# Kernel tuning notes

Measured on AMD Instinct MI355X. Metric: run time of the kernel, lower is better.

The kernel has to match this reference:

```python
import jax, jax.numpy as jnp
import numpy as np

H = 512  # hidden_size


def setup_inputs() -> dict:
    key = jax.random.key(0)
    k1, k2, k3, k4, k5, k6 = jax.random.split(key, 6)
    B, S = 32, 2048
    output = jax.random.normal(k1, (B, H), dtype=jnp.float32)
    encoder_outputs = jax.random.normal(k2, (B, S, 2 * H), dtype=jnp.float32)
    encoder_mask = jax.random.randint(k3, (B, S), 0, 2, dtype=jnp.int32)
    # nn.Linear(3H, H): weight [H, 3H], bias [H]
    bound = 1.0 / np.sqrt(3 * H)
    W_attn = jax.random.uniform(k4, (H, 3 * H), minval=-bound, maxval=bound, dtype=jnp.float32)
    b_attn = jax.random.uniform(k5, (H,), minval=-bound, maxval=bound, dtype=jnp.float32)
    v = jax.random.normal(k6, (H,), dtype=jnp.float32) * (1.0 / np.sqrt(H))
    return {"output": output, "encoder_outputs": encoder_outputs,
            "encoder_mask": encoder_mask, "W_attn": W_attn, "b_attn": b_attn, "v": v}


def reference(output, encoder_outputs, encoder_mask, W_attn, b_attn, v):
    # Equivalent to cat([repeat(output), enc], -1) @ W.T: split W into state/enc blocks
    W_s = W_attn[:, :H]        # [H, H]   acts on decoder state
    W_e = W_attn[:, H:]        # [H, 2H]  acts on encoder outputs
    state_proj = output @ W_s.T                              # [B, H]
    enc_proj = jnp.einsum('bse,he->bsh', encoder_outputs, W_e)  # [B, S, H]
    energy = jnp.tanh(state_proj[:, None, :] + enc_proj + b_attn)  # [B, S, H]
    scores = jnp.einsum('bsh,h->bs', energy, v)[:, None, :]   # [B, 1, S]
    scores = scores - 1000.0 * (encoder_mask[:, None, :] == 0).astype(scores.dtype)
    return jax.nn.softmax(scores, axis=2)
```

## Files before the change

kernel.cpp:

```cpp
#include <hip/hip_runtime.h>
#include <hip/hip_bf16.h>

typedef __attribute__((ext_vector_type(4))) float f32x4;
typedef __attribute__((ext_vector_type(8))) short short8;

#define HH 512
#define BB 32
#define SS 2048
#define KK 1024

__device__ __forceinline__ unsigned short f2bf(float f) {
    unsigned int u = __float_as_uint(f);
    u += 0x7fffu + ((u >> 16) & 1u);
    return (unsigned short)(u >> 16);
}

__device__ __forceinline__ ushort4 pack4(float4 f) {
    ushort4 p;
    p.x = f2bf(f.x); p.y = f2bf(f.y); p.z = f2bf(f.z); p.w = f2bf(f.w);
    return p;
}

__device__ __forceinline__ float fast_tanh(float x) {
    float e = __expf(2.0f * x);
    return 1.0f - 2.0f / (e + 1.0f);
}

__global__ __launch_bounds__(256)
void spb_kernel(const float* __restrict__ out_state,
                const float* __restrict__ W,
                const float* __restrict__ bias,
                float* __restrict__ spb) {
    int wave = threadIdx.x >> 6, lane = threadIdx.x & 63;
    int g = blockIdx.x * 4 + wave;
    int b = g >> 9, h = g & 511;
    const float* wr = W + (size_t)h * 1536;
    const float* ov = out_state + b * HH;
    float4 w0 = *(const float4*)(wr + lane * 8);
    float4 w1 = *(const float4*)(wr + lane * 8 + 4);
    float4 o0 = *(const float4*)(ov + lane * 8);
    float4 o1 = *(const float4*)(ov + lane * 8 + 4);
    float d = w0.x * o0.x + w0.y * o0.y + w0.z * o0.z + w0.w * o0.w
            + w1.x * o1.x + w1.y * o1.y + w1.z * o1.z + w1.w * o1.w;
    d += __shfl_xor(d, 1); d += __shfl_xor(d, 2); d += __shfl_xor(d, 4);
    d += __shfl_xor(d, 8); d += __shfl_xor(d, 16); d += __shfl_xor(d, 32);
    if (lane == 0) spb[g] = d + bias[h];
}

__global__ void wconv_kernel(const float* __restrict__ W, unsigned short* __restrict__ Wt) {
    int idx = blockIdx.x * 256 + threadIdx.x;
    int e8 = idx * 8;
    int h = e8 >> 10;
    int k = e8 & 1023;
    const float* src = W + (size_t)h * 1536 + 512 + k;
    float4 w0 = *(const float4*)src;
    float4 w1 = *(const float4*)(src + 4);
    int kt = k >> 5;
    int q  = (k >> 3) & 3;
    int g  = h >> 4;
    int r  = h & 15;
    int ln = (q << 4) | r;
    unsigned short* dst = Wt + (size_t)kt * 16384 + g * 512 + ln * 8;
    *(ushort4*)dst = pack4(w0);
    *(ushort4*)(dst + 4) = pack4(w1);
}

__global__ __launch_bounds__(512, 4)
void attn_gemm(const float* __restrict__ enc, const unsigned short* __restrict__ Wt,
               const float* __restrict__ spb, const float* __restrict__ vvec,
               float* __restrict__ scores) {
    __shared__ unsigned short Asm[2 * 8192];
    __shared__ float red[8][64];

    const int tid = threadIdx.x;
    const int w = tid >> 6;
    const int lane = tid & 63;
    const int r = lane & 15;
    const int q = lane >> 4;
    const int b = blockIdx.x >> 5;
    const int s0 = (blockIdx.x & 31) << 6;

    const int arow = tid >> 3;
    const int akq = tid & 7;
    const float* arowp = enc + ((size_t)(b * SS + s0 + arow)) * KK + akq * 4;
    const int st_off = tid * 4;
    const int rd_off = r * 32 + q * 8;
    const unsigned short* wbase = Wt + (size_t)w * 2048 + lane * 8;

    f32x4 acc[4][4] = {};
    float4 f[4];

    #pragma unroll
    for (int t = 0; t < 4; ++t) f[t] = *(const float4*)(arowp + t * 32);
    #pragma unroll
    for (int t = 0; t < 4; ++t)
        *(ushort4*)(Asm + t * 2048 + st_off) = pack4(f[t]);
    __syncthreads();

    for (int p = 0; p < 8; ++p) {
        const int buf = p & 1;
        if (p < 7) {
            const float* src = arowp + (p + 1) * 128;
            #pragma unroll
            for (int t = 0; t < 4; ++t) f[t] = *(const float4*)(src + t * 32);
        }
        #pragma unroll
        for (int sub = 0; sub < 4; ++sub) {
            const int kt = p * 4 + sub;
            const short8* wp = (const short8*)(wbase + (size_t)kt * 16384);
            short8 bf[4];
            #pragma unroll
            for (int nf = 0; nf < 4; ++nf) bf[nf] = wp[nf * 64];
            const short8* ap = (const short8*)(Asm + buf * 8192 + sub * 2048 + rd_off);
            short8 af[4];
            #pragma unroll
            for (int mt = 0; mt < 4; ++mt) af[mt] = ap[mt * 64];
            #pragma unroll
            for (int mt = 0; mt < 4; ++mt)
                #pragma unroll
                for (int nf = 0; nf < 4; ++nf)
                    acc[mt][nf] = __builtin_amdgcn_mfma_f32_16x16x32_bf16(
                        af[mt], bf[nf], acc[mt][nf], 0, 0, 0);
        }
        if (p < 7) {
            unsigned short* dst = Asm + (buf ^ 1) * 8192 + st_off;
            #pragma unroll
            for (int t = 0; t < 4; ++t)
                *(ushort4*)(dst + t * 2048) = pack4(f[t]);
            __syncthreads();
        }
    }

    float vh[4], sh[4];
    #pragma unroll
    for (int nf = 0; nf < 4; ++nf) {
        int h = w * 64 + nf * 16 + r;
        vh[nf] = vvec[h];
        sh[nf] = spb[b * HH + h];
    }
    float rowacc[4][4] = {};
    #pragma unroll
    for (int mt = 0; mt < 4; ++mt)
        #pragma unroll
        for (int nf = 0; nf < 4; ++nf)
            #pragma unroll
            for (int i = 0; i < 4; ++i) {
                float x = acc[mt][nf][i] + sh[nf];
                rowacc[mt][i] += vh[nf] * fast_tanh(x);
            }
    #pragma unroll
    for (int mt = 0; mt < 4; ++mt)
        #pragma unroll
        for (int i = 0; i < 4; ++i) {
            float t = rowacc[mt][i];
            t += __shfl_xor(t, 1);
            t += __shfl_xor(t, 2);
            t += __shfl_xor(t, 4);
            t += __shfl_xor(t, 8);
            rowacc[mt][i] = t;
        }
    if (r == 0) {
        #pragma unroll
        for (int mt = 0; mt < 4; ++mt)
            #pragma unroll
            for (int i = 0; i < 4; ++i)
                red[w][mt * 16 + q * 4 + i] = rowacc[mt][i];
    }
    __syncthreads();
    if (tid < 64) {
        float sum = 0.f;
        #pragma unroll
        for (int ww = 0; ww < 8; ++ww) sum += red[ww][tid];
        scores[b * SS + s0 + tid] = sum;
    }
}

__global__ void softmax_kernel(const float* __restrict__ scores,
                               const int* __restrict__ mask,
                               float* __restrict__ out) {
    __shared__ float red[256];
    int b = blockIdx.x, tid = threadIdx.x;
    float x[8];
    #pragma unroll
    for (int i = 0; i < 8; ++i) {
        int s = tid + i * 256;
        float sc = scores[b * SS + s];
        if (mask[b * SS + s] == 0) sc -= 1000.0f;
        x[i] = sc;
    }
    float mx = x[0];
    #pragma unroll
    for (int i = 1; i < 8; ++i) mx = fmaxf(mx, x[i]);
    red[tid] = mx;
    __syncthreads();
    for (int o = 128; o > 0; o >>= 1) {
        if (tid < o) red[tid] = fmaxf(red[tid], red[tid + o]);
        __syncthreads();
    }
    mx = red[0];
    __syncthreads();
    float e[8], sum = 0.f;
    #pragma unroll
    for (int i = 0; i < 8; ++i) { e[i] = __expf(x[i] - mx); sum += e[i]; }
    red[tid] = sum;
    __syncthreads();
    for (int o = 128; o > 0; o >>= 1) {
        if (tid < o) red[tid] += red[tid + o];
        __syncthreads();
    }
    float inv = 1.0f / red[0];
    #pragma unroll
    for (int i = 0; i < 8; ++i) out[b * SS + tid + i * 256] = e[i] * inv;
}

extern "C" void kernel_launch(void* const* d_in, const int* in_sizes, int n_in,
                              void* d_out, int out_size, void* d_ws, size_t ws_size,
                              hipStream_t stream) {
    const float* out_state = (const float*)d_in[0];
    const float* enc       = (const float*)d_in[1];
    const int*   mask      = (const int*)d_in[2];
    const float* W_attn    = (const float*)d_in[3];
    const float* b_attn    = (const float*)d_in[4];
    const float* vvec      = (const float*)d_in[5];
    float* out = (float*)d_out;

    char* ws = (char*)d_ws;
    float*          spb    = (float*)ws;
    unsigned short* Wt     = (unsigned short*)(ws + 65536);
    float*          scores = (float*)(ws + 65536 + 1048576);

    spb_kernel<<<4096, 256, 0, stream>>>(out_state, W_attn, b_attn, spb);
    wconv_kernel<<<256, 256, 0, stream>>>(W_attn, Wt);
    attn_gemm<<<1024, 512, 0, stream>>>(enc, Wt, spb, vvec, scores);
    softmax_kernel<<<32, 256, 0, stream>>>(scores, mask, out);
}
```

Before: 429.1 us.

## Stage weight tiles in LDS via async global-to-LDS copies with swizzled A tile

The GEMM now loads the bf16 weight tiles into shared memory with asynchronous global_load_lds copies, so each block fetches each weight tile once instead of every wave reading weights straight from global memory. The K loop is reorganised into 32 single-step iterations with double-buffered A and B tiles. An XOR swizzle is applied to the A tile layout to reduce LDS bank conflicts. In exchange there are many more barriers (one per 32-wide K step), a larger LDS footprint that may lower occupancy, and smaller prefetch granularity for the encoder activations.

```diff
diff --git a/kernel.cpp b/kernel.cpp
--- a/kernel.cpp
+++ b/kernel.cpp
@@ -24,6 +24,12 @@
 __device__ __forceinline__ float fast_tanh(float x) {
     float e = __expf(2.0f * x);
     return 1.0f - 2.0f / (e + 1.0f);
+}
+
+__device__ __forceinline__ void async_copy16(const void* g, void* l) {
+    __builtin_amdgcn_global_load_lds(
+        (__attribute__((address_space(1))) const void*)g,
+        (__attribute__((address_space(3))) void*)l, 16, 0, 0);
 }
 
 __global__ __launch_bounds__(256)
@@ -69,7 +75,8 @@
 void attn_gemm(const float* __restrict__ enc, const unsigned short* __restrict__ Wt,
                const float* __restrict__ spb, const float* __restrict__ vvec,
                float* __restrict__ scores) {
-    __shared__ unsigned short Asm[2 * 8192];
+    __shared__ __align__(16) unsigned short Asm[2][2048];
+    __shared__ __align__(16) unsigned short Bsm[2][16384];
     __shared__ float red[8][64];
 
     const int tid = threadIdx.x;
@@ -81,54 +88,54 @@
     const int s0 = (blockIdx.x & 31) << 6;
 
     const int arow = tid >> 3;
-    const int akq = tid & 7;
-    const float* arowp = enc + ((size_t)(b * SS + s0 + arow)) * KK + akq * 4;
-    const int st_off = tid * 4;
-    const int rd_off = r * 32 + q * 8;
-    const unsigned short* wbase = Wt + (size_t)w * 2048 + lane * 8;
+    const int akq  = tid & 7;
+    const float* asrc = enc + ((size_t)(b * SS + s0 + arow)) * KK + akq * 4;
+    const int akey = (arow ^ (arow >> 2)) & 3;
+    const int ast  = arow * 32 + ((((akq >> 1) ^ akey) << 3) | ((akq & 1) << 2));
+
+    const unsigned short* bsrc = Wt + tid * 8;
+
+    const int rkey = (r ^ (r >> 2)) & 3;
+    const int ard  = r * 32 + ((q ^ rkey) << 3);
+    const int brd  = (w * 4) * 512 + lane * 8;
 
     f32x4 acc[4][4] = {};
-    float4 f[4];
-
-    #pragma unroll
-    for (int t = 0; t < 4; ++t) f[t] = *(const float4*)(arowp + t * 32);
-    #pragma unroll
-    for (int t = 0; t < 4; ++t)
-        *(ushort4*)(Asm + t * 2048 + st_off) = pack4(f[t]);
-    __syncthreads();
-
-    for (int p = 0; p < 8; ++p) {
+
+    {
+        float4 f0 = *(const float4*)asrc;
+        #pragma unroll
+        for (int c = 0; c < 4; ++c)
+            async_copy16(bsrc + c * 4096, &Bsm[0][c * 4096 + tid * 8]);
+        *(ushort4*)&Asm[0][ast] = pack4(f0);
+    }
+    __syncthreads();
+
+    for (int p = 0; p < 32; ++p) {
         const int buf = p & 1;
-        if (p < 7) {
-            const float* src = arowp + (p + 1) * 128;
-            #pragma unroll
-            for (int t = 0; t < 4; ++t) f[t] = *(const float4*)(src + t * 32);
+        float4 f;
+        if (p < 31) {
+            f = *(const float4*)(asrc + (p + 1) * 32);
+            const unsigned short* src = bsrc + (size_t)(p + 1) * 16384;
+            #pragma unroll
+            for (int c = 0; c < 4; ++c)
+                async_copy16(src + c * 4096, &Bsm[buf ^ 1][c * 4096 + tid * 8]);
         }
-        #pragma unroll
-        for (int sub = 0; sub < 4; ++sub) {
-            const int kt = p * 4 + sub;
-            const short8* wp = (const short8*)(wbase + (size_t)kt * 16384);
-            short8 bf[4];
-            #pragma unroll
-            for (int nf = 0; nf < 4; ++nf) bf[nf] = wp[nf * 64];
-            const short8* ap = (const short8*)(Asm + buf * 8192 + sub * 2048 + rd_off);
-            short8 af[4];
-            #pragma unroll
-            for (int mt = 0; mt < 4; ++mt) af[mt] = ap[mt * 64];
-            #pragma unroll
-            for (int mt = 0; mt < 4; ++mt)
-                #pragma unroll
-                for (int nf = 0; nf < 4; ++nf)
-                    acc[mt][nf] = __builtin_amdgcn_mfma_f32_16x16x32_bf16(
-                        af[mt], bf[nf], acc[mt][nf], 0, 0, 0);
-        }
-        if (p < 7) {
-            unsigned short* dst = Asm + (buf ^ 1) * 8192 + st_off;
-            #pragma unroll
-            for (int t = 0; t < 4; ++t)
-                *(ushort4*)(dst + t * 2048) = pack4(f[t]);
-            __syncthreads();
-        }
+        short8 af[4], bf[4];
+        #pragma unroll
+        for (int mt = 0; mt < 4; ++mt)
+            af[mt] = *(const short8*)&Asm[buf][mt * 512 + ard];
+        #pragma unroll
+        for (int nf = 0; nf < 4; ++nf)
+            bf[nf] = *(const short8*)&Bsm[buf][nf * 512 + brd];
+        #pragma unroll
+        for (int mt = 0; mt < 4; ++mt)
+            #pragma unroll
+            for (int nf = 0; nf < 4; ++nf)
+                acc[mt][nf] = __builtin_amdgcn_mfma_f32_16x16x32_bf16(
+                    af[mt], bf[nf], acc[mt][nf], 0, 0, 0);
+        if (p < 31)
+            *(ushort4*)&Asm[buf ^ 1][ast] = pack4(f);
+        __syncthreads();
     }
 
     float vh[4], sh[4];
```

Result: slower. 445.6 us (+3.8%).

## Load A fragments directly from global into registers, doubling rows per block

Applied to the files above, without the earlier changes.

The GEMM no longer stages encoder rows through LDS with double buffering and barriers. Each lane now loads its MFMA A-fragment straight from global memory, converts it to bf16 in registers and prefetches the next k-slice. Each block covers 128 rows instead of 64, so the weight fragments loaded per wave are reused across twice as many rows, and launch bounds drop to 2 blocks per SM. The costs are more register pressure and lower occupancy, and the global loads per lane are 32-byte pieces spread across rows, which may coalesce less well than the old row-contiguous staging.

```diff
diff --git a/kernel.cpp b/kernel.cpp
--- a/kernel.cpp
+++ b/kernel.cpp
@@ -24,6 +24,20 @@
 __device__ __forceinline__ float fast_tanh(float x) {
     float e = __expf(2.0f * x);
     return 1.0f - 2.0f / (e + 1.0f);
+}
+
+__device__ __forceinline__ short8 cvt_bf8(const float4& a0, const float4& a1) {
+    short8 o;
+    union { __hip_bfloat16 h; unsigned short u; } c;
+    c.h = __float2bfloat16(a0.x); o[0] = (short)c.u;
+    c.h = __float2bfloat16(a0.y); o[1] = (short)c.u;
+    c.h = __float2bfloat16(a0.z); o[2] = (short)c.u;
+    c.h = __float2bfloat16(a0.w); o[3] = (short)c.u;
+    c.h = __float2bfloat16(a1.x); o[4] = (short)c.u;
+    c.h = __float2bfloat16(a1.y); o[5] = (short)c.u;
+    c.h = __float2bfloat16(a1.z); o[6] = (short)c.u;
+    c.h = __float2bfloat16(a1.w); o[7] = (short)c.u;
+    return o;
 }
 
 __global__ __launch_bounds__(256)
@@ -65,69 +79,80 @@
     *(ushort4*)(dst + 4) = pack4(w1);
 }
 
-__global__ __launch_bounds__(512, 4)
+__global__ __launch_bounds__(512, 2)
 void attn_gemm(const float* __restrict__ enc, const unsigned short* __restrict__ Wt,
                const float* __restrict__ spb, const float* __restrict__ vvec,
                float* __restrict__ scores) {
-    __shared__ unsigned short Asm[2 * 8192];
-    __shared__ float red[8][64];
+    __shared__ float red[8][128];
 
     const int tid = threadIdx.x;
     const int w = tid >> 6;
     const int lane = tid & 63;
     const int r = lane & 15;
     const int q = lane >> 4;
-    const int b = blockIdx.x >> 5;
-    const int s0 = (blockIdx.x & 31) << 6;
-
-    const int arow = tid >> 3;
-    const int akq = tid & 7;
-    const float* arowp = enc + ((size_t)(b * SS + s0 + arow)) * KK + akq * 4;
-    const int st_off = tid * 4;
-    const int rd_off = r * 32 + q * 8;
-    const unsigned short* wbase = Wt + (size_t)w * 2048 + lane * 8;
-
-    f32x4 acc[4][4] = {};
-    float4 f[4];
-
-    #pragma unroll
-    for (int t = 0; t < 4; ++t) f[t] = *(const float4*)(arowp + t * 32);
-    #pragma unroll
-    for (int t = 0; t < 4; ++t)
-        *(ushort4*)(Asm + t * 2048 + st_off) = pack4(f[t]);
-    __syncthreads();
-
-    for (int p = 0; p < 8; ++p) {
-        const int buf = p & 1;
-        if (p < 7) {
-            const float* src = arowp + (p + 1) * 128;
-            #pragma unroll
-            for (int t = 0; t < 4; ++t) f[t] = *(const float4*)(src + t * 32);
-        }
-        #pragma unroll
-        for (int sub = 0; sub < 4; ++sub) {
-            const int kt = p * 4 + sub;
-            const short8* wp = (const short8*)(wbase + (size_t)kt * 16384);
-            short8 bf[4];
-            #pragma unroll
-            for (int nf = 0; nf < 4; ++nf) bf[nf] = wp[nf * 64];
-            const short8* ap = (const short8*)(Asm + buf * 8192 + sub * 2048 + rd_off);
-            short8 af[4];
-            #pragma unroll
-            for (int mt = 0; mt < 4; ++mt) af[mt] = ap[mt * 64];
+    const int b = blockIdx.x >> 4;
+    const int s0 = (blockIdx.x & 15) << 7;
+    const int bS = b * SS + s0;
+
+    const float* aP[8];
+    #pragma unroll
+    for (int mt = 0; mt < 8; ++mt)
+        aP[mt] = enc + (size_t)(bS + mt * 16 + r) * KK + q * 8;
+
+    const short8* wp = (const short8*)Wt + (size_t)(w * 4) * 64 + lane;
+
+    f32x4 acc[8][4] = {};
+    float4 fA[8][2];
+    short8 bfr[4];
+
+    #pragma unroll
+    for (int mt = 0; mt < 8; ++mt) {
+        fA[mt][0] = *(const float4*)(aP[mt]);
+        fA[mt][1] = *(const float4*)(aP[mt] + 4);
+    }
+    #pragma unroll
+    for (int nf = 0; nf < 4; ++nf) bfr[nf] = wp[nf * 64];
+
+    #pragma unroll 1
+    for (int kt = 0; kt < 32; ++kt) {
+        const int kadv = (kt + 1) * 32;
+        short8 af[4];
+
+        #pragma unroll
+        for (int mt = 0; mt < 4; ++mt)
+            af[mt] = cvt_bf8(fA[mt][0], fA[mt][1]);
+        if (kt < 31) {
+            #pragma unroll
+            for (int mt = 0; mt < 4; ++mt) {
+                fA[mt][0] = *(const float4*)(aP[mt] + kadv);
+                fA[mt][1] = *(const float4*)(aP[mt] + kadv + 4);
+            }
+        }
+        #pragma unroll
+        for (int nf = 0; nf < 4; ++nf)
             #pragma unroll
             for (int mt = 0; mt < 4; ++mt)
-                #pragma unroll
-                for (int nf = 0; nf < 4; ++nf)
-                    acc[mt][nf] = __builtin_amdgcn_mfma_f32_16x16x32_bf16(
-                        af[mt], bf[nf], acc[mt][nf], 0, 0, 0);
-        }
-        if (p < 7) {
-            unsigned short* dst = Asm + (buf ^ 1) * 8192 + st_off;
-            #pragma unroll
-            for (int t = 0; t < 4; ++t)
-                *(ushort4*)(dst + t * 2048) = pack4(f[t]);
-            __syncthreads();
+                acc[mt][nf] = __builtin_amdgcn_mfma_f32_16x16x32_bf16(
+                    af[mt], bfr[nf], acc[mt][nf], 0, 0, 0);
+
+        #pragma unroll
+        for (int mt = 0; mt < 4; ++mt)
+            af[mt] = cvt_bf8(fA[mt + 4][0], fA[mt + 4][1]);
+        if (kt < 31) {
+            #pragma unroll
+            for (int mt = 0; mt < 4; ++mt) {
+                fA[mt + 4][0] = *(const float4*)(aP[mt + 4] + kadv);
+                fA[mt + 4][1] = *(const float4*)(aP[mt + 4] + kadv + 4);
+            }
+        }
+        #pragma unroll
+        for (int nf = 0; nf < 4; ++nf) {
+            #pragma unroll
+            for (int mt = 0; mt < 4; ++mt)
+                acc[mt + 4][nf] = __builtin_amdgcn_mfma_f32_16x16x32_bf16(
+                    af[mt], bfr[nf], acc[mt + 4][nf], 0, 0, 0);
+            if (kt < 31)
+                bfr[nf] = wp[(size_t)(kt + 1) * 2048 + nf * 64];
         }
     }
 
@@ -138,9 +163,9 @@
         vh[nf] = vvec[h];
         sh[nf] = spb[b * HH + h];
     }
-    float rowacc[4][4] = {};
-    #pragma unroll
-    for (int mt = 0; mt < 4; ++mt)
+    float rowacc[8][4] = {};
+    #pragma unroll
+    for (int mt = 0; mt < 8; ++mt)
         #pragma unroll
         for (int nf = 0; nf < 4; ++nf)
             #pragma unroll
@@ -149,7 +174,7 @@
                 rowacc[mt][i] += vh[nf] * fast_tanh(x);
             }
     #pragma unroll
-    for (int mt = 0; mt < 4; ++mt)
+    for (int mt = 0; mt < 8; ++mt)
         #pragma unroll
         for (int i = 0; i < 4; ++i) {
             float t = rowacc[mt][i];
@@ -161,17 +186,17 @@
         }
     if (r == 0) {
         #pragma unroll
-        for (int mt = 0; mt < 4; ++mt)
+        for (int mt = 0; mt < 8; ++mt)
             #pragma unroll
             for (int i = 0; i < 4; ++i)
                 red[w][mt * 16 + q * 4 + i] = rowacc[mt][i];
     }
     __syncthreads();
-    if (tid < 64) {
+    if (tid < 128) {
         float sum = 0.f;
         #pragma unroll
         for (int ww = 0; ww < 8; ++ww) sum += red[ww][tid];
-        scores[b * SS + s0 + tid] = sum;
+        scores[bS + tid] = sum;
     }
 }
 
@@ -231,6 +256,6 @@
 
     spb_kernel<<<4096, 256, 0, stream>>>(out_state, W_attn, b_attn, spb);
     wconv_kernel<<<256, 256, 0, stream>>>(W_attn, Wt);
-    attn_gemm<<<1024, 512, 0, stream>>>(enc, Wt, spb, vvec, scores);
+    attn_gemm<<<512, 512, 0, stream>>>(enc, Wt, spb, vvec, scores);
     softmax_kernel<<<32, 256, 0, stream>>>(scores, mask, out);
 }
```

Result: slower. 567.2 us (+32.2%).
